# Kernel tuning notes

Measured on AMD Instinct MI355X. Metric: run time of the kernel, lower is better.

The kernel has to match this reference:

```python
import jax, jax.numpy as jnp
import numpy as np

NUM_ROT = 8
OUT_CH = 128
IN_CH = 128
KSIZE = 3


def _resample(filt, angle):
    """Rotate a (O, I, k, k) filter bank by `angle` via bilinear resampling,
    matching F.affine_grid/F.grid_sample with align_corners=True, zero padding."""
    k = filt.shape[-1]
    c, s = jnp.cos(angle), jnp.sin(angle)
    lin = jnp.linspace(-1.0, 1.0, k)
    gy, gx = jnp.meshgrid(lin, lin, indexing='ij')  # (k, k) output coords
    # theta = [[c, -s, 0], [s, c, 0]] applied to (x, y, 1)
    xs = c * gx - s * gy
    ys = s * gx + c * gy
    ix = (xs + 1.0) * 0.5 * (k - 1)  # normalized -> pixel coords
    iy = (ys + 1.0) * 0.5 * (k - 1)
    x0f, y0f = jnp.floor(ix), jnp.floor(iy)
    x0, y0 = x0f.astype(jnp.int32), y0f.astype(jnp.int32)
    wx, wy = ix - x0f, iy - y0f

    def tap(yi, xi, w):
        valid = ((yi >= 0) & (yi < k) & (xi >= 0) & (xi < k)).astype(filt.dtype)
        yc = jnp.clip(yi, 0, k - 1)
        xc = jnp.clip(xi, 0, k - 1)
        return filt[:, :, yc, xc] * (valid * w)  # (O, I, k, k)

    return (tap(y0, x0, (1 - wy) * (1 - wx)) + tap(y0, x0 + 1, (1 - wy) * wx)
            + tap(y0 + 1, x0, wy * (1 - wx)) + tap(y0 + 1, x0 + 1, wy * wx))


def setup_inputs() -> dict:
    key = jax.random.key(0)
    k1, k2, k3 = jax.random.split(key, 3)
    x = jax.random.normal(k1, (16, IN_CH, 128, 128), jnp.float32)
    # base_conv.weight: (out_channels * num_rotations, in_channels, k, k)
    weight = jax.random.normal(k2, (OUT_CH * NUM_ROT, IN_CH, KSIZE, KSIZE), jnp.float32) * 0.05
    rot_alpha = jax.random.normal(k3, (NUM_ROT,), jnp.float32) * 0.1 + 1.0
    return {"x": x, "weight": weight, "rot_alpha": rot_alpha}


def reference(x, weight, rot_alpha):
    R, O, K = NUM_ROT, OUT_CH, KSIZE
    # weight.view(O, R, I, K, K)[:, i] per rotation -> (R, O, I, K, K)
    w_r = weight.reshape(O, R, -1, K, K).transpose(1, 0, 2, 3, 4)
    angles = rot_alpha * (jnp.pi / 4) * jnp.arange(R, dtype=jnp.float32)
    rot_w = jax.vmap(_resample)(w_r, angles)  # (R, O, I, K, K)
    filters = rot_w.reshape(R * O, -1, K, K)
    # one conv with all rotated filter banks instead of R separate convs
    y = jax.lax.conv_general_dilated(
        x, filters, window_strides=(1, 1),
        padding=[(K // 2, K // 2), (K // 2, K // 2)],
        dimension_numbers=('NCHW', 'OIHW', 'NCHW'))  # (B, R*O, H, W)
    B, _, H, W = y.shape
    return y.reshape(B, R, O, H, W).max(axis=1)  # max over rotations
```

## Files before the change

kernel.cpp:

```cpp
#include <hip/hip_runtime.h>

typedef short short8 __attribute__((ext_vector_type(8)));
typedef float f32x4 __attribute__((ext_vector_type(4)));

#define XP_BYTES (16ull * 130 * 130 * 128 * 2)

static __device__ __forceinline__ unsigned short f2bf(float f) {
  unsigned u = __float_as_uint(f);
  u += 0x7FFFu + ((u >> 16) & 1u);
  return (unsigned short)(u >> 16);
}

static __device__ __forceinline__ void gload16(const void* g, void* l) {
  __builtin_amdgcn_global_load_lds(
      (const __attribute__((address_space(1))) void*)g,
      (__attribute__((address_space(3))) void*)l, 16, 0, 0);
}

static __device__ __forceinline__ float wtap(const float* f, int yi, int xi) {
  bool valid = (yi >= 0) & (yi < 3) & (xi >= 0) & (xi < 3);
  int yc = min(max(yi, 0), 2), xc = min(max(xi, 0), 2);
  return valid ? f[yc * 3 + xc] : 0.f;
}

__global__ __launch_bounds__(256) void wprep_kernel(
    const float* __restrict__ w, const float* __restrict__ rot_alpha,
    unsigned short* __restrict__ w2) {
  int gid = blockIdx.x * 256 + threadIdx.x;
  int ic = gid & 127;
  int nr = gid >> 7;
  int r = nr & 7;
  const float* wf = w + (size_t)nr * (128 * 9) + (size_t)ic * 9;
  float f[9];
#pragma unroll
  for (int q = 0; q < 9; ++q) f[q] = wf[q];
  float ang = rot_alpha[r] * 0.78539816339744830962f * (float)r;
  float sth, cth;
  sincosf(ang, &sth, &cth);
#pragma unroll
  for (int j = 0; j < 3; ++j) {
#pragma unroll
    for (int i = 0; i < 3; ++i) {
      float gy = (float)(j - 1), gx = (float)(i - 1);
      float xs = cth * gx - sth * gy;
      float ys = sth * gx + cth * gy;
      float ix = xs + 1.0f, iy = ys + 1.0f;
      float x0f = floorf(ix), y0f = floorf(iy);
      int x0 = (int)x0f, y0 = (int)y0f;
      float wx = ix - x0f, wy = iy - y0f;
      float acc = wtap(f, y0, x0) * (1.f - wy) * (1.f - wx)
                + wtap(f, y0, x0 + 1) * (1.f - wy) * wx
                + wtap(f, y0 + 1, x0) * wy * (1.f - wx)
                + wtap(f, y0 + 1, x0 + 1) * wy * wx;
      w2[(size_t)nr * 1152 + (size_t)(j * 3 + i) * 128 + ic] = f2bf(acc);
    }
  }
}

__global__ __launch_bounds__(256) void xprep_kernel(
    const float* __restrict__ x, unsigned short* __restrict__ xp) {
  const int yy = blockIdx.x;
  const int b = blockIdx.y;
  const int t = threadIdx.x;
  const size_t rowbase = ((size_t)b * 130 + yy) * (130 * 128);
  if (yy == 0 || yy == 129) {
    uint4 z = {0u, 0u, 0u, 0u};
    for (int i = t; i < 2080; i += 256)
      ((uint4*)(xp + rowbase))[i] = z;
    return;
  }
  const int y = yy - 1;
  __shared__ float lt[32][129];
  if (t < 32) {
    uint4 z = {0u, 0u, 0u, 0u};
    int xx = (t < 16) ? 0 : 129;
    int cc = (t & 15) * 8;
    *(uint4*)(xp + rowbase + (size_t)xx * 128 + cc) = z;
  }
  for (int c0 = 0; c0 < 128; c0 += 32) {
#pragma unroll
    for (int i = 0; i < 16; ++i) {
      int idx = i * 256 + t;
      int c = idx >> 7, wq = idx & 127;
      lt[c][wq] = x[(((size_t)b * 128 + c0 + c) * 128 + y) * 128 + wq];
    }
    __syncthreads();
#pragma unroll
    for (int i = 0; i < 2; ++i) {
      int u = i * 256 + t;
      int xx = u >> 2, cp = (u & 3) * 8;
      unsigned short v[8];
#pragma unroll
      for (int q = 0; q < 8; ++q) v[q] = f2bf(lt[cp + q][xx]);
      *(uint4*)(xp + rowbase + (size_t)(xx + 1) * 128 + c0 + cp) = *(uint4*)v;
    }
    __syncthreads();
  }
}

__global__ __launch_bounds__(512, 2) void conv_kernel(
    const unsigned short* __restrict__ xp,
    const unsigned short* __restrict__ w2,
    float* __restrict__ out) {
  __shared__ unsigned short lds[65536];

  const int tid = threadIdx.x;
  const int lane = tid & 63;
  const int wv = tid >> 6;
  const int wr = wv >> 2;
  const int wc = wv & 3;

  const int bid = blockIdx.x;
  const int wg = (bid & 7) * 512 + (bid >> 3);
  const int mblk = wg >> 2;
  const int nblk = wg & 3;
  const int b = mblk >> 6;
  const int y0 = (mblk & 63) << 1;

  const int r0 = tid >> 2;
  const int s0 = tid & 3;
  const int g0 = s0 ^ ((r0 >> 1) & 3);
  const int wvoff = wv * 512;

  const unsigned short* xpt =
      xp + (size_t)(b * 130 + y0) * 130 * 128 + r0 * 128 + g0 * 8;
  const unsigned short* wpt =
      w2 + (size_t)nblk * 256 * 1152 + (size_t)r0 * 1152 + g0 * 8;

  const int l15 = lane & 15;
  const int lhi = lane >> 4;
  const int sa = (lhi ^ ((l15 >> 1) & 3)) * 8;

  const int aRd = wr * 8192 + l15 * 32 + sa;
  const int bRd = 32768 + (wc >> 1) * 8192 + (wc & 1) * 2048 + l15 * 32 + sa;

  f32x4 acc[8][4];
#pragma unroll
  for (int mf = 0; mf < 8; ++mf)
#pragma unroll
    for (int nf = 0; nf < 4; ++nf) acc[mf][nf] = (f32x4){0.f, 0.f, 0.f, 0.f};

#define STAGE_A(BUF, HP, KK, DY, DX, CH)                                     \
  gload16(xpt + ((HP + DY) * 130 + DX) * 128 + (CH) * 64 + (KK) * 32,        \
          lds + (BUF) * 16384 + (HP) * 8192 + (KK) * 4096 + wvoff)
#define STAGE_B(BUF, HN, KK, TAP, CH)                                        \
  gload16(wpt + (size_t)(HN) * 147456 + (TAP) * 128 + (CH) * 64 + (KK) * 32, \
          lds + 32768 + (BUF) * 16384 + (HN) * 8192 + (KK) * 4096 + wvoff)

  STAGE_A(0, 0, 0, 0, 0, 0);
  STAGE_A(0, 1, 0, 0, 0, 0);
  STAGE_B(0, 0, 0, 0, 0);
  STAGE_B(0, 1, 0, 0, 0);
  STAGE_A(0, 0, 1, 0, 0, 0);
  STAGE_A(0, 1, 1, 0, 0, 0);
  STAGE_B(0, 0, 1, 0, 0);
  STAGE_B(0, 1, 1, 0, 0);
  asm volatile("s_waitcnt vmcnt(4)" ::: "memory");
  __builtin_amdgcn_s_barrier();

#pragma unroll 2
  for (int kt = 0; kt < 18; ++kt) {
    const int buf = kt & 1;
    const bool st = kt < 17;
    const int nt = kt + 1;
    const int ntap = nt >> 1;
    const int nch = nt & 1;
    const int nbuf = nt & 1;
    const int ndy = ntap / 3;
    const int ndx = ntap - ndy * 3;

    const unsigned short* pA = lds + buf * 16384 + aRd;
    const unsigned short* pB = lds + buf * 16384 + bRd;
    short8 af[4], bf[4];

#pragma unroll
    for (int q = 0; q < 4; ++q) af[q] = *(const short8*)(pA + q * 512);
#pragma unroll
    for (int nf = 0; nf < 4; ++nf) bf[nf] = *(const short8*)(pB + nf * 512);
    if (st) { STAGE_A(nbuf, 0, 0, ndy, ndx, nch); STAGE_A(nbuf, 1, 0, ndy, ndx, nch); }
    __builtin_amdgcn_s_barrier();
    asm volatile("s_waitcnt lgkmcnt(0)" ::: "memory");
    __builtin_amdgcn_s_setprio(1);
#pragma unroll
    for (int q = 0; q < 4; ++q)
#pragma unroll
      for (int nf = 0; nf < 4; ++nf)
        acc[q][nf] = __builtin_amdgcn_mfma_f32_16x16x32_bf16(af[q], bf[nf],
                                                             acc[q][nf], 0, 0, 0);
    __builtin_amdgcn_s_setprio(0);
    __builtin_amdgcn_s_barrier();

#pragma unroll
    for (int q = 0; q < 4; ++q) af[q] = *(const short8*)(pA + 2048 + q * 512);
    if (st) { STAGE_B(nbuf, 0, 0, ntap, nch); STAGE_B(nbuf, 1, 0, ntap, nch); }
    if (st) asm volatile("s_waitcnt vmcnt(4)" ::: "memory");
    else    asm volatile("s_waitcnt vmcnt(0)" ::: "memory");
    __builtin_amdgcn_s_barrier();
    asm volatile("s_waitcnt lgkmcnt(0)" ::: "memory");
    __builtin_amdgcn_s_setprio(1);
#pragma unroll
    for (int q = 0; q < 4; ++q)
#pragma unroll
      for (int nf = 0; nf < 4; ++nf)
        acc[4 + q][nf] = __builtin_amdgcn_mfma_f32_16x16x32_bf16(
            af[q], bf[nf], acc[4 + q][nf], 0, 0, 0);
    __builtin_amdgcn_s_setprio(0);
    __builtin_amdgcn_s_barrier();

#pragma unroll
    for (int q = 0; q < 4; ++q) af[q] = *(const short8*)(pA + 4096 + q * 512);
#pragma unroll
    for (int nf = 0; nf < 4; ++nf) bf[nf] = *(const short8*)(pB + 4096 + nf * 512);
    if (st) { STAGE_A(nbuf, 0, 1, ndy, ndx, nch); STAGE_A(nbuf, 1, 1, ndy, ndx, nch); }
    __builtin_amdgcn_s_barrier();
    asm volatile("s_waitcnt lgkmcnt(0)" ::: "memory");
    __builtin_amdgcn_s_setprio(1);
#pragma unroll
    for (int q = 0; q < 4; ++q)
#pragma unroll
      for (int nf = 0; nf < 4; ++nf)
        acc[q][nf] = __builtin_amdgcn_mfma_f32_16x16x32_bf16(af[q], bf[nf],
                                                             acc[q][nf], 0, 0, 0);
    __builtin_amdgcn_s_setprio(0);
    __builtin_amdgcn_s_barrier();

#pragma unroll
    for (int q = 0; q < 4; ++q)
      af[q] = *(const short8*)(pA + 4096 + 2048 + q * 512);
    if (st) { STAGE_B(nbuf, 0, 1, ntap, nch); STAGE_B(nbuf, 1, 1, ntap, nch); }
    if (st) asm volatile("s_waitcnt vmcnt(4)" ::: "memory");
    else    asm volatile("s_waitcnt vmcnt(0)" ::: "memory");
    __builtin_amdgcn_s_barrier();
    asm volatile("s_waitcnt lgkmcnt(0)" ::: "memory");
    __builtin_amdgcn_s_setprio(1);
#pragma unroll
    for (int q = 0; q < 4; ++q)
#pragma unroll
      for (int nf = 0; nf < 4; ++nf)
        acc[4 + q][nf] = __builtin_amdgcn_mfma_f32_16x16x32_bf16(
            af[q], bf[nf], acc[4 + q][nf], 0, 0, 0);
    __builtin_amdgcn_s_setprio(0);
    __builtin_amdgcn_s_barrier();
  }
#undef STAGE_A
#undef STAGE_B

  float* lE = (float*)lds;
#pragma unroll
  for (int mf = 0; mf < 8; ++mf)
#pragma unroll
    for (int nf = 0; nf < 4; ++nf)
#pragma unroll
      for (int j = 0; j < 4; ++j) {
        float v = acc[mf][nf][j];
        v = fmaxf(v, __shfl_xor(v, 1, 64));
        v = fmaxf(v, __shfl_xor(v, 2, 64));
        v = fmaxf(v, __shfl_xor(v, 4, 64));
        if ((lane & 7) == 0) {
          int pix = wr * 128 + mf * 16 + lhi * 4 + j;
          int ol = wc * 8 + nf * 2 + ((lane >> 3) & 1);
          lE[pix * 33 + ol] = v;
        }
      }
  __syncthreads();
  const size_t obase = ((size_t)(b * 128 + nblk * 32) * 128 + y0) * 128;
#pragma unroll
  for (int i = 0; i < 16; ++i) {
    int idx = i * 512 + tid;
    int ol = idx >> 8;
    int pix = idx & 255;
    int yl = pix >> 7;
    int xx = pix & 127;
    out[obase + (size_t)ol * 16384 + yl * 128 + xx] = lE[pix * 33 + ol];
  }
}

extern "C" void kernel_launch(void* const* d_in, const int* in_sizes, int n_in,
                              void* d_out, int out_size, void* d_ws, size_t ws_size,
                              hipStream_t stream) {
  const float* x = (const float*)d_in[0];
  const float* w = (const float*)d_in[1];
  const float* ra = (const float*)d_in[2];
  float* out = (float*)d_out;
  unsigned short* xp = (unsigned short*)d_ws;
  unsigned short* w2 = (unsigned short*)((char*)d_ws + XP_BYTES);

  hipLaunchKernelGGL(wprep_kernel, dim3(512), dim3(256), 0, stream, w, ra, w2);
  hipLaunchKernelGGL(xprep_kernel, dim3(130, 16), dim3(256), 0, stream, x, xp);
  hipLaunchKernelGGL(conv_kernel, dim3(4096), dim3(512), 0, stream, xp, w2, out);
}
```

Measured before the change: 766.5 us.

## Double-buffer MFMA operand registers to overlap LDS reads with MFMA compute

```diff
diff --git a/kernel.cpp b/kernel.cpp
--- a/kernel.cpp
+++ b/kernel.cpp
@@ -147,6 +147,8 @@
   gload16(wpt + (size_t)(HN) * 147456 + (TAP) * 128 + (CH) * 64 + (KK) * 32, \
           lds + 32768 + (BUF) * 16384 + (HN) * 8192 + (KK) * 4096 + wvoff)
 
+  short8 af0[4], af1[4], bf0[4], bf1[4];
+
   STAGE_A(0, 0, 0, 0, 0, 0);
   STAGE_A(0, 1, 0, 0, 0, 0);
   STAGE_B(0, 0, 0, 0, 0);
@@ -157,88 +159,89 @@
   STAGE_B(0, 1, 1, 0, 0);
   asm volatile("s_waitcnt vmcnt(4)" ::: "memory");
   __builtin_amdgcn_s_barrier();
+  {
+    const unsigned short* pA = lds + aRd;
+    const unsigned short* pB = lds + bRd;
+#pragma unroll
+    for (int q = 0; q < 4; ++q) af0[q] = *(const short8*)(pA + q * 512);
+#pragma unroll
+    for (int nf = 0; nf < 4; ++nf) bf0[nf] = *(const short8*)(pB + nf * 512);
+  }
 
 #pragma unroll 2
   for (int kt = 0; kt < 18; ++kt) {
     const int buf = kt & 1;
+    const int nbuf = buf ^ 1;
     const bool st = kt < 17;
     const int nt = kt + 1;
     const int ntap = nt >> 1;
     const int nch = nt & 1;
-    const int nbuf = nt & 1;
     const int ndy = ntap / 3;
     const int ndx = ntap - ndy * 3;
 
     const unsigned short* pA = lds + buf * 16384 + aRd;
     const unsigned short* pB = lds + buf * 16384 + bRd;
-    short8 af[4], bf[4];
-
-#pragma unroll
-    for (int q = 0; q < 4; ++q) af[q] = *(const short8*)(pA + q * 512);
-#pragma unroll
-    for (int nf = 0; nf < 4; ++nf) bf[nf] = *(const short8*)(pB + nf * 512);
+    const unsigned short* pAn = lds + nbuf * 16384 + aRd;
+    const unsigned short* pBn = lds + nbuf * 16384 + bRd;
+
     if (st) { STAGE_A(nbuf, 0, 0, ndy, ndx, nch); STAGE_A(nbuf, 1, 0, ndy, ndx, nch); }
-    __builtin_amdgcn_s_barrier();
-    asm volatile("s_waitcnt lgkmcnt(0)" ::: "memory");
-    __builtin_amdgcn_s_setprio(1);
-#pragma unroll
-    for (int q = 0; q < 4; ++q)
-#pragma unroll
-      for (int nf = 0; nf < 4; ++nf)
-        acc[q][nf] = __builtin_amdgcn_mfma_f32_16x16x32_bf16(af[q], bf[nf],
+#pragma unroll
+    for (int q = 0; q < 4; ++q) af1[q] = *(const short8*)(pA + 2048 + q * 512);
+    __builtin_amdgcn_s_setprio(1);
+#pragma unroll
+    for (int q = 0; q < 4; ++q)
+#pragma unroll
+      for (int nf = 0; nf < 4; ++nf)
+        acc[q][nf] = __builtin_amdgcn_mfma_f32_16x16x32_bf16(af0[q], bf0[nf],
                                                              acc[q][nf], 0, 0, 0);
     __builtin_amdgcn_s_setprio(0);
-    __builtin_amdgcn_s_barrier();
-
-#pragma unroll
-    for (int q = 0; q < 4; ++q) af[q] = *(const short8*)(pA + 2048 + q * 512);
+    asm volatile("s_waitcnt vmcnt(2)" ::: "memory");
+    __builtin_amdgcn_s_barrier();
+
     if (st) { STAGE_B(nbuf, 0, 0, ntap, nch); STAGE_B(nbuf, 1, 0, ntap, nch); }
-    if (st) asm volatile("s_waitcnt vmcnt(4)" ::: "memory");
-    else    asm volatile("s_waitcnt vmcnt(0)" ::: "memory");
-    __builtin_amdgcn_s_barrier();
-    asm volatile("s_waitcnt lgkmcnt(0)" ::: "memory");
+#pragma unroll
+    for (int q = 0; q < 4; ++q) af0[q] = *(const short8*)(pA + 4096 + q * 512);
+#pragma unroll
+    for (int nf = 0; nf < 4; ++nf) bf1[nf] = *(const short8*)(pB + 4096 + nf * 512);
     __builtin_amdgcn_s_setprio(1);
 #pragma unroll
     for (int q = 0; q < 4; ++q)
 #pragma unroll
       for (int nf = 0; nf < 4; ++nf)
         acc[4 + q][nf] = __builtin_amdgcn_mfma_f32_16x16x32_bf16(
-            af[q], bf[nf], acc[4 + q][nf], 0, 0, 0);
-    __builtin_amdgcn_s_setprio(0);
-    __builtin_amdgcn_s_barrier();
-
-#pragma unroll
-    for (int q = 0; q < 4; ++q) af[q] = *(const short8*)(pA + 4096 + q * 512);
-#pragma unroll
-    for (int nf = 0; nf < 4; ++nf) bf[nf] = *(const short8*)(pB + 4096 + nf * 512);
+            af1[q], bf0[nf], acc[4 + q][nf], 0, 0, 0);
+    __builtin_amdgcn_s_setprio(0);
+    __builtin_amdgcn_s_barrier();
+
     if (st) { STAGE_A(nbuf, 0, 1, ndy, ndx, nch); STAGE_A(nbuf, 1, 1, ndy, ndx, nch); }
-    __builtin_amdgcn_s_barrier();
-    asm volatile("s_waitcnt lgkmcnt(0)" ::: "memory");
-    __builtin_amdgcn_s_setprio(1);
-#pragma unroll
-    for (int q = 0; q < 4; ++q)
-#pragma unroll
-      for (int nf = 0; nf < 4; ++nf)
-        acc[q][nf] = __builtin_amdgcn_mfma_f32_16x16x32_bf16(af[q], bf[nf],
+#pragma unroll
+    for (int q = 0; q < 4; ++q)
+      af1[q] = *(const short8*)(pA + 4096 + 2048 + q * 512);
+    __builtin_amdgcn_s_setprio(1);
+#pragma unroll
+    for (int q = 0; q < 4; ++q)
+#pragma unroll
+      for (int nf = 0; nf < 4; ++nf)
+        acc[q][nf] = __builtin_amdgcn_mfma_f32_16x16x32_bf16(af0[q], bf1[nf],
                                                              acc[q][nf], 0, 0, 0);
     __builtin_amdgcn_s_setprio(0);
-    __builtin_amdgcn_s_barrier();
-
-#pragma unroll
-    for (int q = 0; q < 4; ++q)
-      af[q] = *(const short8*)(pA + 4096 + 2048 + q * 512);
+    asm volatile("s_waitcnt vmcnt(2)" ::: "memory");
+    __builtin_amdgcn_s_barrier();
+
     if (st) { STAGE_B(nbuf, 0, 1, ntap, nch); STAGE_B(nbuf, 1, 1, ntap, nch); }
-    if (st) asm volatile("s_waitcnt vmcnt(4)" ::: "memory");
-    else    asm volatile("s_waitcnt vmcnt(0)" ::: "memory");
-    __builtin_amdgcn_s_barrier();
-    asm volatile("s_waitcnt lgkmcnt(0)" ::: "memory");
+    if (st) {
+#pragma unroll
+      for (int q = 0; q < 4; ++q) af0[q] = *(const short8*)(pAn + q * 512);
+#pragma unroll
+      for (int nf = 0; nf < 4; ++nf) bf0[nf] = *(const short8*)(pBn + nf * 512);
+    }
     __builtin_amdgcn_s_setprio(1);
 #pragma unroll
     for (int q = 0; q < 4; ++q)
 #pragma unroll
       for (int nf = 0; nf < 4; ++nf)
         acc[4 + q][nf] = __builtin_amdgcn_mfma_f32_16x16x32_bf16(
-            af[q], bf[nf], acc[4 + q][nf], 0, 0, 0);
+            af1[q], bf1[nf], acc[4 + q][nf], 0, 0, 0);
     __builtin_amdgcn_s_setprio(0);
     __builtin_amdgcn_s_barrier();
   }
```

New measurement: 963.5 us. 1.26x slower.
